# Performance work log

Measured on AMD Instinct MI355X. Metric: run time of the kernel, lower is better.

## Reference

```python
import jax, jax.numpy as jnp
import numpy as np

N = 50000      # nodes
E = 800000     # edges
IN = 128       # in_channels
H = 128        # hidden_channels
OUT = 500      # out_channels
EPS = 1e-5


def setup_inputs() -> dict:
    key = jax.random.key(0)
    ks = jax.random.split(key, 8)
    def rn(k, shape, scale=0.05):
        return jax.random.normal(k, shape, jnp.float32) * scale
    return {
        "x": jax.random.normal(ks[0], (N, IN), jnp.float32),
        "edge_index": jax.random.randint(ks[1], (2, E), 0, N, dtype=jnp.int32),
        "W1": rn(ks[2], (IN, H)), "b1": jnp.zeros((H,), jnp.float32),
        "g1": jnp.ones((H,), jnp.float32), "be1": jnp.zeros((H,), jnp.float32),
        "W2": rn(ks[3], (H, 2 * H)), "b2": jnp.zeros((2 * H,), jnp.float32),
        "g2": jnp.ones((2 * H,), jnp.float32), "be2": jnp.zeros((2 * H,), jnp.float32),
        "W3": rn(ks[4], (2 * H, H)), "b3": jnp.zeros((H,), jnp.float32),
        "g3": jnp.ones((H,), jnp.float32), "be3": jnp.zeros((H,), jnp.float32),
        "Wl1": rn(ks[5], (H, H // 2)), "bl1": jnp.zeros((H // 2,), jnp.float32),
        "g4": jnp.ones((H // 2,), jnp.float32), "be4": jnp.zeros((H // 2,), jnp.float32),
        "Wl2": rn(ks[6], (H // 2, OUT)), "bl2": jnp.zeros((OUT,), jnp.float32),
    }


def layer_norm(x, g, b):
    mu = jnp.mean(x, axis=-1, keepdims=True)
    var = jnp.mean(jnp.square(x - mu), axis=-1, keepdims=True)
    return (x - mu) * jax.lax.rsqrt(var + EPS) * g + b


def gcn_conv(x, W, b, src, dst, n):
    # PyG GCNConv: x' = D^{-1/2} (A + I) D^{-1/2} (x W) + b, with self-loops.
    h = x @ W                                   # [N, F]
    ones = jnp.ones(src.shape[0], h.dtype)
    deg = jax.ops.segment_sum(ones, dst, num_segments=n) + 1.0  # +1 self-loop
    dinv = jnp.where(deg > 0, jax.lax.rsqrt(deg), 0.0)          # [N]
    coef = dinv[src] * dinv[dst]                # [E]
    agg = jax.ops.segment_sum(h[src] * coef[:, None], dst, num_segments=n)
    agg = agg + h * jnp.square(dinv)[:, None]   # self-loop messages
    return agg + b


def reference(x, edge_index, W1, b1, g1, be1, W2, b2, g2, be2,
              W3, b3, g3, be3, Wl1, bl1, g4, be4, Wl2, bl2):
    # eval mode: dropout is identity
    src, dst = edge_index[0], edge_index[1]
    n = x.shape[0]
    h = jax.nn.elu(layer_norm(gcn_conv(x, W1, b1, src, dst, n), g1, be1))
    h = jax.nn.elu(layer_norm(gcn_conv(h, W2, b2, src, dst, n), g2, be2))
    h = jax.nn.elu(layer_norm(gcn_conv(h, W3, b3, src, dst, n), g3, be3))
    h = jax.nn.elu(layer_norm(h @ Wl1 + bl1, g4, be4))
    return h @ Wl2 + bl2
```

## Files before the change

### kernel.cpp

```cpp
#include <hip/hip_runtime.h>
#include <cstdint>


#define LN_EPS 1e-5f

typedef __attribute__((ext_vector_type(8))) short bf16x8;
typedef __attribute__((ext_vector_type(4))) float f32x4;

static __device__ __forceinline__ ushort f2bf(float f) {
  union { float f; uint u; } c; c.f = f;
  uint u = c.u;
  return (ushort)((u + 0x7fffu + ((u >> 16) & 1u)) >> 16);
}
static __device__ __forceinline__ float bf2f(ushort h) {
  union { uint u; float f; } c; c.u = (uint)h << 16;
  return c.f;
}


__global__ void zero1_kernel(int* __restrict__ a, int n) {
  int i = blockIdx.x * blockDim.x + threadIdx.x;
  if (i < n) a[i] = 0;
}

__global__ void deg_kernel(const int* __restrict__ dst, int* __restrict__ deg, int E) {
  int e = blockIdx.x * blockDim.x + threadIdx.x;
  if (e < E) atomicAdd(&deg[dst[e]], 1);
}

__global__ void scan1_kernel(const int* __restrict__ deg, int* __restrict__ excl,
                             int* __restrict__ bsums, float* __restrict__ dinv, int N) {
  __shared__ int s[256];
  int tid = threadIdx.x;
  int i = blockIdx.x * 256 + tid;
  int v = (i < N) ? deg[i] : 0;
  s[tid] = v;
  __syncthreads();
  for (int o = 1; o < 256; o <<= 1) {
    int t = (tid >= o) ? s[tid - o] : 0;
    __syncthreads();
    if (tid >= o) s[tid] += t;
    __syncthreads();
  }
  if (i < N) {
    excl[i] = s[tid] - v;
    dinv[i] = rsqrtf((float)v + 1.0f);
  }
  if (tid == 255) bsums[blockIdx.x] = s[tid];
}

__global__ void scan2_kernel(int* __restrict__ bsums, int nb) {
  __shared__ int s[256];
  int tid = threadIdx.x;
  int v = (tid < nb) ? bsums[tid] : 0;
  s[tid] = v;
  __syncthreads();
  for (int o = 1; o < 256; o <<= 1) {
    int t = (tid >= o) ? s[tid - o] : 0;
    __syncthreads();
    if (tid >= o) s[tid] += t;
    __syncthreads();
  }
  if (tid < nb) bsums[tid] = s[tid] - v;
}

__global__ void scan3_kernel(int* __restrict__ rowptr, int* __restrict__ fill,
                             const int* __restrict__ bsums, int N, int Etotal) {
  int i = blockIdx.x * blockDim.x + threadIdx.x;
  if (i < N) {
    int v = rowptr[i] + bsums[i >> 8];
    rowptr[i] = v;
    fill[i] = v;
  } else if (i == N) {
    rowptr[N] = Etotal;
  }
}

__global__ void fill_kernel(const int* __restrict__ src, const int* __restrict__ dst,
                            int* __restrict__ fill, int* __restrict__ srcs, int E) {
  int e = blockIdx.x * blockDim.x + threadIdx.x;
  if (e >= E) return;
  int idx = atomicAdd(&fill[dst[e]], 1);
  srcs[idx] = src[e];
}


__global__ void f2bf_vec_kernel(const float* __restrict__ in, ushort* __restrict__ out, int n4) {
  int i = blockIdx.x * blockDim.x + threadIdx.x;
  if (i >= n4) return;
  float4 v = ((const float4*)in)[i];
  ushort4 o;
  o.x = f2bf(v.x); o.y = f2bf(v.y); o.z = f2bf(v.z); o.w = f2bf(v.w);
  ((ushort4*)out)[i] = o;
}

struct WConvArgs {
  const float* w[5];
  ushort* wt[5];
  int K[5], N[5];
  int off[6];
};

__global__ void wconv_kernel(WConvArgs a, int total) {
  int i = blockIdx.x * blockDim.x + threadIdx.x;
  if (i >= total) return;
  int m = 0;
  while (i >= a.off[m + 1]) m++;
  int j = i - a.off[m];
  int k = j / a.N[m], n = j - k * a.N[m];
  a.wt[m][(size_t)n * a.K[m] + k] = f2bf(a.w[m][j]);
}

#define TBM 128
#define TBN 128
#define TBK 32
#define LDK 40

template <bool OUT_BF16>
__global__ __launch_bounds__(256, 2) void mfma_gemm_kernel(
    const ushort* __restrict__ A, const ushort* __restrict__ Bt,
    const float* __restrict__ bias, void* __restrict__ Cout,
    int M, int N, int K) {
  __shared__ ushort As[TBM][LDK];
  __shared__ ushort Bs[TBN][LDK];
  const int tid = threadIdx.x;
  const int lane = tid & 63;
  const int w = tid >> 6;
  const int wm = w & 1, wn = w >> 1;
  const int quad = lane >> 4, l16 = lane & 15;
  const int rowBase = blockIdx.y * TBM;
  const int colBase = blockIdx.x * TBN;

  f32x4 acc[4][4] = {};
  const int lr = tid >> 2;
  const int lk = (tid & 3) * 8;

  for (int k0 = 0; k0 < K; k0 += TBK) {
#pragma unroll
    for (int h = 0; h < 2; h++) {
      int r = lr + h * 64;
      int grow = rowBase + r;
      uint4 va = make_uint4(0, 0, 0, 0);
      if (grow < M) va = *(const uint4*)(A + (size_t)grow * K + k0 + lk);
      *(uint4*)&As[r][lk] = va;
      int gcol = colBase + r;
      uint4 vb = make_uint4(0, 0, 0, 0);
      if (gcol < N) vb = *(const uint4*)(Bt + (size_t)gcol * K + k0 + lk);
      *(uint4*)&Bs[r][lk] = vb;
    }
    __syncthreads();
    bf16x8 af[4], bfr[4];
#pragma unroll
    for (int i = 0; i < 4; i++) {
      af[i]  = *(const bf16x8*)&As[wm * 64 + i * 16 + l16][quad * 8];
      bfr[i] = *(const bf16x8*)&Bs[wn * 64 + i * 16 + l16][quad * 8];
    }
#pragma unroll
    for (int i = 0; i < 4; i++)
#pragma unroll
      for (int j = 0; j < 4; j++)
        acc[i][j] = __builtin_amdgcn_mfma_f32_16x16x32_bf16(af[i], bfr[j], acc[i][j], 0, 0, 0);
    __syncthreads();
  }
#pragma unroll
  for (int i = 0; i < 4; i++) {
    int row0 = rowBase + wm * 64 + i * 16 + quad * 4;
#pragma unroll
    for (int j = 0; j < 4; j++) {
      int col = colBase + wn * 64 + j * 16 + l16;
      if (col >= N) continue;
      float bv = bias ? bias[col] : 0.f;
#pragma unroll
      for (int r = 0; r < 4; r++) {
        int row = row0 + r;
        if (row >= M) continue;
        float v = acc[i][j][r] + bv;
        if (OUT_BF16) ((ushort*)Cout)[(size_t)row * N + col] = f2bf(v);
        else          ((float*)Cout)[(size_t)row * N + col] = v;
      }
    }
  }
}


__global__ __launch_bounds__(256) void agg_kernel(
    const ushort* __restrict__ hb, const int* __restrict__ rowptr,
    const int* __restrict__ srcs, const float* __restrict__ dinv,
    uint* __restrict__ out, int Nn) {
  const int wave = threadIdx.x >> 6;
  const int n = blockIdx.x * 4 + wave;
  if (n >= Nn) return;
  const int f = threadIdx.x & 63;
  const uint* h32 = (const uint*)hb;
  const float di = dinv[n];
  uint self = h32[(size_t)n * 64 + f];
  float a0 = bf2f((ushort)(self & 0xffffu)) * di * di;
  float a1 = bf2f((ushort)(self >> 16)) * di * di;
  int i = rowptr[n];
  const int e = rowptr[n + 1];
  for (; i + 3 < e; i += 4) {
    int s0 = srcs[i], s1 = srcs[i + 1], s2 = srcs[i + 2], s3 = srcs[i + 3];
    float c0 = dinv[s0] * di, c1 = dinv[s1] * di, c2 = dinv[s2] * di, c3 = dinv[s3] * di;
    uint v0 = h32[(size_t)s0 * 64 + f];
    uint v1 = h32[(size_t)s1 * 64 + f];
    uint v2 = h32[(size_t)s2 * 64 + f];
    uint v3 = h32[(size_t)s3 * 64 + f];
    a0 += c0 * bf2f((ushort)(v0 & 0xffffu)) + c1 * bf2f((ushort)(v1 & 0xffffu)) +
          c2 * bf2f((ushort)(v2 & 0xffffu)) + c3 * bf2f((ushort)(v3 & 0xffffu));
    a1 += c0 * bf2f((ushort)(v0 >> 16)) + c1 * bf2f((ushort)(v1 >> 16)) +
          c2 * bf2f((ushort)(v2 >> 16)) + c3 * bf2f((ushort)(v3 >> 16));
  }
  for (; i < e; i++) {
    int s = srcs[i];
    float c = dinv[s] * di;
    uint v = h32[(size_t)s * 64 + f];
    a0 += c * bf2f((ushort)(v & 0xffffu));
    a1 += c * bf2f((ushort)(v >> 16));
  }
  out[(size_t)n * 64 + f] = (uint)f2bf(a0) | ((uint)f2bf(a1) << 16);
}

__global__ __launch_bounds__(256) void agg_ln_kernel(
    const ushort* __restrict__ hb, const int* __restrict__ rowptr,
    const int* __restrict__ srcs, const float* __restrict__ dinv,
    const float* __restrict__ bias, const float* __restrict__ g,
    const float* __restrict__ be, uint* __restrict__ out, int Nn) {
  const int wave = threadIdx.x >> 6;
  const int n = blockIdx.x * 4 + wave;
  if (n >= Nn) return;
  const int f = threadIdx.x & 63;
  const uint* h32 = (const uint*)hb;
  const float di = dinv[n];
  uint self = h32[(size_t)n * 64 + f];
  float2 bv = ((const float2*)bias)[f];
  float a0 = bf2f((ushort)(self & 0xffffu)) * di * di + bv.x;
  float a1 = bf2f((ushort)(self >> 16)) * di * di + bv.y;
  int i = rowptr[n];
  const int e = rowptr[n + 1];
  for (; i + 3 < e; i += 4) {
    int s0 = srcs[i], s1 = srcs[i + 1], s2 = srcs[i + 2], s3 = srcs[i + 3];
    float c0 = dinv[s0] * di, c1 = dinv[s1] * di, c2 = dinv[s2] * di, c3 = dinv[s3] * di;
    uint v0 = h32[(size_t)s0 * 64 + f];
    uint v1 = h32[(size_t)s1 * 64 + f];
    uint v2 = h32[(size_t)s2 * 64 + f];
    uint v3 = h32[(size_t)s3 * 64 + f];
    a0 += c0 * bf2f((ushort)(v0 & 0xffffu)) + c1 * bf2f((ushort)(v1 & 0xffffu)) +
          c2 * bf2f((ushort)(v2 & 0xffffu)) + c3 * bf2f((ushort)(v3 & 0xffffu));
    a1 += c0 * bf2f((ushort)(v0 >> 16)) + c1 * bf2f((ushort)(v1 >> 16)) +
          c2 * bf2f((ushort)(v2 >> 16)) + c3 * bf2f((ushort)(v3 >> 16));
  }
  for (; i < e; i++) {
    int s = srcs[i];
    float c = dinv[s] * di;
    uint v = h32[(size_t)s * 64 + f];
    a0 += c * bf2f((ushort)(v & 0xffffu));
    a1 += c * bf2f((ushort)(v >> 16));
  }
  float s = a0 + a1;
#pragma unroll
  for (int o = 32; o >= 1; o >>= 1) s += __shfl_xor(s, o);
  float mean = s * (1.0f / 128.0f);
  float d0 = a0 - mean, d1 = a1 - mean;
  float q = d0 * d0 + d1 * d1;
#pragma unroll
  for (int o = 32; o >= 1; o >>= 1) q += __shfl_xor(q, o);
  float rstd = rsqrtf(q * (1.0f / 128.0f) + LN_EPS);
  float2 gv = ((const float2*)g)[f];
  float2 bev = ((const float2*)be)[f];
  float y0 = d0 * rstd * gv.x + bev.x;
  float y1 = d1 * rstd * gv.y + bev.y;
  y0 = (y0 > 0.f) ? y0 : expm1f(y0);
  y1 = (y1 > 0.f) ? y1 : expm1f(y1);
  out[(size_t)n * 64 + f] = (uint)f2bf(y0) | ((uint)f2bf(y1) << 16);
}

template <int F, bool IN_BF16>
__global__ __launch_bounds__(F) void ln_elu_kernel(const void* __restrict__ xin,
                                                   const float* __restrict__ g,
                                                   const float* __restrict__ be,
                                                   ushort* __restrict__ out) {
  constexpr int NW = (F + 63) / 64;
  __shared__ float sb[NW];
  const int row = blockIdx.x;
  const int f = threadIdx.x;
  float v;
  if (IN_BF16) v = bf2f(((const ushort*)xin)[(size_t)row * F + f]);
  else         v = ((const float*)xin)[(size_t)row * F + f];
  float s = v;
#pragma unroll
  for (int o = 32; o >= 1; o >>= 1) s += __shfl_xor(s, o);
  float mean;
  if constexpr (NW == 1) {
    mean = s * (1.0f / F);
  } else {
    if ((f & 63) == 0) sb[f >> 6] = s;
    __syncthreads();
    float t = 0.f;
#pragma unroll
    for (int w2 = 0; w2 < NW; w2++) t += sb[w2];
    mean = t * (1.0f / F);
    __syncthreads();
  }
  float d = v - mean;
  float q = d * d;
#pragma unroll
  for (int o = 32; o >= 1; o >>= 1) q += __shfl_xor(q, o);
  float var;
  if constexpr (NW == 1) {
    var = q * (1.0f / F);
  } else {
    if ((f & 63) == 0) sb[f >> 6] = q;
    __syncthreads();
    float t = 0.f;
#pragma unroll
    for (int w2 = 0; w2 < NW; w2++) t += sb[w2];
    var = t * (1.0f / F);
  }
  float y = d * rsqrtf(var + LN_EPS) * g[f] + be[f];
  out[(size_t)row * F + f] = f2bf((y > 0.f) ? y : expm1f(y));
}


extern "C" void kernel_launch(void* const* d_in, const int* in_sizes, int n_in,
                              void* d_out, int out_size, void* d_ws, size_t ws_size,
                              hipStream_t stream) {
  const float* x   = (const float*)d_in[0];
  const int*   ei  = (const int*)d_in[1];
  const float* W1  = (const float*)d_in[2];
  const float* b1  = (const float*)d_in[3];
  const float* g1  = (const float*)d_in[4];
  const float* be1 = (const float*)d_in[5];
  const float* W2  = (const float*)d_in[6];
  const float* b2  = (const float*)d_in[7];
  const float* g2  = (const float*)d_in[8];
  const float* be2 = (const float*)d_in[9];
  const float* W3  = (const float*)d_in[10];
  const float* b3  = (const float*)d_in[11];
  const float* g3  = (const float*)d_in[12];
  const float* be3 = (const float*)d_in[13];
  const float* Wl1 = (const float*)d_in[14];
  const float* bl1 = (const float*)d_in[15];
  const float* g4  = (const float*)d_in[16];
  const float* be4 = (const float*)d_in[17];
  const float* Wl2 = (const float*)d_in[18];
  const float* bl2 = (const float*)d_in[19];

  const int N = in_sizes[0] / 128;
  const int E = in_sizes[1] / 2;
  const int* esrc = ei;
  const int* edst = ei + E;

  char* p = (char*)d_ws;
  float* F1 = (float*)p;              p += (size_t)N * 128 * 4;
  ushort* Pb = (ushort*)p;            p += (size_t)N * 256 * 2;
  ushort* Qb = (ushort*)p;            p += (size_t)N * 256 * 2;
  ushort* W1t = (ushort*)p;           p += 128 * 128 * 2;
  ushort* W2t = (ushort*)p;           p += 128 * 256 * 2;
  ushort* W3t = (ushort*)p;           p += 256 * 128 * 2;
  ushort* Wl1t = (ushort*)p;          p += 128 * 64 * 2;
  ushort* Wl2t = (ushort*)p;          p += 64 * 500 * 2;
  int*   srcs  = (int*)p;             p += (size_t)E * 4;
  int*   deg   = (int*)p;             p += (size_t)N * 4;
  float* dinv  = (float*)p;           p += (size_t)N * 4;
  int*   rowptr= (int*)p;             p += (size_t)(N + 2) * 4;
  int*   fill  = (int*)p;             p += (size_t)N * 4;
  int*   bsums = (int*)p;             p += 256 * 4;
  ushort* xb = (ushort*)F1;

  const int nb = (N + 255) / 256;
  const int eb = (E + 255) / 256;

  zero1_kernel<<<nb, 256, 0, stream>>>(deg, N);
  deg_kernel<<<eb, 256, 0, stream>>>(edst, deg, E);
  scan1_kernel<<<nb, 256, 0, stream>>>(deg, rowptr, bsums, dinv, N);
  scan2_kernel<<<1, 256, 0, stream>>>(bsums, nb);
  scan3_kernel<<<(N + 256) / 256, 256, 0, stream>>>(rowptr, fill, bsums, N, E);
  fill_kernel<<<eb, 256, 0, stream>>>(esrc, edst, fill, srcs, E);

  f2bf_vec_kernel<<<(N * 128 / 4 + 255) / 256, 256, 0, stream>>>(x, xb, N * 128 / 4);
  WConvArgs wa;
  wa.w[0] = W1;  wa.wt[0] = W1t;  wa.K[0] = 128; wa.N[0] = 128;
  wa.w[1] = W2;  wa.wt[1] = W2t;  wa.K[1] = 128; wa.N[1] = 256;
  wa.w[2] = W3;  wa.wt[2] = W3t;  wa.K[2] = 256; wa.N[2] = 128;
  wa.w[3] = Wl1; wa.wt[3] = Wl1t; wa.K[3] = 128; wa.N[3] = 64;
  wa.w[4] = Wl2; wa.wt[4] = Wl2t; wa.K[4] = 64;  wa.N[4] = 500;
  wa.off[0] = 0;
  for (int m = 0; m < 5; m++) wa.off[m + 1] = wa.off[m] + wa.K[m] * wa.N[m];
  int wtotal = wa.off[5];
  wconv_kernel<<<(wtotal + 255) / 256, 256, 0, stream>>>(wa, wtotal);

  auto gemm_bf = [&](const ushort* A, const ushort* Bt, const float* bias, ushort* C,
                     int M, int Nn, int K) {
    dim3 grid((Nn + TBN - 1) / TBN, (M + TBM - 1) / TBM);
    mfma_gemm_kernel<true><<<grid, 256, 0, stream>>>(A, Bt, bias, C, M, Nn, K);
  };
  auto gemm_f32 = [&](const ushort* A, const ushort* Bt, const float* bias, float* C,
                      int M, int Nn, int K) {
    dim3 grid((Nn + TBN - 1) / TBN, (M + TBM - 1) / TBM);
    mfma_gemm_kernel<false><<<grid, 256, 0, stream>>>(A, Bt, bias, C, M, Nn, K);
  };
  const int ab = (N + 3) / 4;

  gemm_bf(xb, W1t, nullptr, Pb, N, 128, 128);
  agg_ln_kernel<<<ab, 256, 0, stream>>>(Pb, rowptr, srcs, dinv, b1, g1, be1, (uint*)Qb, N);

  agg_kernel<<<ab, 256, 0, stream>>>(Qb, rowptr, srcs, dinv, (uint*)Pb, N);
  gemm_bf(Pb, W2t, b2, Qb, N, 256, 128);
  ln_elu_kernel<256, true><<<N, 256, 0, stream>>>(Qb, g2, be2, Pb);

  gemm_bf(Pb, W3t, nullptr, Qb, N, 128, 256);
  agg_ln_kernel<<<ab, 256, 0, stream>>>(Qb, rowptr, srcs, dinv, b3, g3, be3, (uint*)Pb, N);

  gemm_f32(Pb, Wl1t, bl1, F1, N, 64, 128);
  ln_elu_kernel<64, false><<<N, 64, 0, stream>>>(F1, g4, be4, Qb);

  gemm_f32(Qb, Wl2t, bl2, (float*)d_out, N, 500, 64);
}
```

Before: 531.0 us.

## Fuse input bf16 cast, LN-ELU epilogue, and scan/zero kernels to cut launches

The first GEMM now reads fp32 x directly and converts to bf16 while staging tiles, which removes the separate conversion kernel and its round trip through memory. The Wl1 GEMM gets a fused LayerNorm+ELU epilogue (64 columns, reduced with 16-lane shuffles), so the fp32 intermediate and the separate ln_elu kernel are gone. The degree zeroing is folded into the weight-conversion kernel, and scan2/scan3 are merged into one kernel in which each block reduces the preceding block sums itself. Together these cut kernel launches and intermediate traffic, at the cost of redundant per-block reductions and half of the waves sitting idle in the fused epilogue.

Measured after the change: 518.7 us. 2.3% less time.

```diff
diff --git a/kernel.cpp b/kernel.cpp
--- a/kernel.cpp
+++ b/kernel.cpp
@@ -17,11 +17,6 @@
   return c.f;
 }
 
-
-__global__ void zero1_kernel(int* __restrict__ a, int n) {
-  int i = blockIdx.x * blockDim.x + threadIdx.x;
-  if (i < n) a[i] = 0;
-}
 
 __global__ void deg_kernel(const int* __restrict__ dst, int* __restrict__ deg, int E) {
   int e = blockIdx.x * blockDim.x + threadIdx.x;
@@ -49,28 +44,24 @@
   if (tid == 255) bsums[blockIdx.x] = s[tid];
 }
 
-__global__ void scan2_kernel(int* __restrict__ bsums, int nb) {
-  __shared__ int s[256];
-  int tid = threadIdx.x;
-  int v = (tid < nb) ? bsums[tid] : 0;
-  s[tid] = v;
+__global__ void scan23_kernel(int* __restrict__ rowptr, int* __restrict__ fill,
+                              const int* __restrict__ bsums, int N, int Etotal, int nb) {
+  __shared__ int sh[256];
+  const int tid = threadIdx.x;
+  const int bix = blockIdx.x;
+  int v = (tid < bix && tid < nb) ? bsums[tid] : 0;
+  sh[tid] = v;
   __syncthreads();
-  for (int o = 1; o < 256; o <<= 1) {
-    int t = (tid >= o) ? s[tid - o] : 0;
-    __syncthreads();
-    if (tid >= o) s[tid] += t;
-    __syncthreads();
-  }
-  if (tid < nb) bsums[tid] = s[tid] - v;
-}
-
-__global__ void scan3_kernel(int* __restrict__ rowptr, int* __restrict__ fill,
-                             const int* __restrict__ bsums, int N, int Etotal) {
-  int i = blockIdx.x * blockDim.x + threadIdx.x;
+  for (int o = 128; o > 0; o >>= 1) {
+    if (tid < o) sh[tid] += sh[tid + o];
+    __syncthreads();
+  }
+  const int off = sh[0];
+  int i = bix * 256 + tid;
   if (i < N) {
-    int v = rowptr[i] + bsums[i >> 8];
-    rowptr[i] = v;
-    fill[i] = v;
+    int r = rowptr[i] + off;
+    rowptr[i] = r;
+    fill[i] = r;
   } else if (i == N) {
     rowptr[N] = Etotal;
   }
@@ -85,15 +76,6 @@
 }
 
 
-__global__ void f2bf_vec_kernel(const float* __restrict__ in, ushort* __restrict__ out, int n4) {
-  int i = blockIdx.x * blockDim.x + threadIdx.x;
-  if (i >= n4) return;
-  float4 v = ((const float4*)in)[i];
-  ushort4 o;
-  o.x = f2bf(v.x); o.y = f2bf(v.y); o.z = f2bf(v.z); o.w = f2bf(v.w);
-  ((ushort4*)out)[i] = o;
-}
-
 struct WConvArgs {
   const float* w[5];
   ushort* wt[5];
@@ -101,8 +83,9 @@
   int off[6];
 };
 
-__global__ void wconv_kernel(WConvArgs a, int total) {
+__global__ void prep_kernel(WConvArgs a, int total, int* __restrict__ deg, int Nn) {
   int i = blockIdx.x * blockDim.x + threadIdx.x;
+  if (i < Nn) deg[i] = 0;
   if (i >= total) return;
   int m = 0;
   while (i >= a.off[m + 1]) m++;
@@ -116,10 +99,11 @@
 #define TBK 32
 #define LDK 40
 
-template <bool OUT_BF16>
+template <int AF32, int EMODE>
 __global__ __launch_bounds__(256, 2) void mfma_gemm_kernel(
-    const ushort* __restrict__ A, const ushort* __restrict__ Bt,
-    const float* __restrict__ bias, void* __restrict__ Cout,
+    const void* __restrict__ A, const ushort* __restrict__ Bt,
+    const float* __restrict__ bias, const float* __restrict__ gamma,
+    const float* __restrict__ beta, void* __restrict__ Cout,
     int M, int N, int K) {
   __shared__ ushort As[TBM][LDK];
   __shared__ ushort Bs[TBN][LDK];
@@ -140,9 +124,26 @@
     for (int h = 0; h < 2; h++) {
       int r = lr + h * 64;
       int grow = rowBase + r;
-      uint4 va = make_uint4(0, 0, 0, 0);
-      if (grow < M) va = *(const uint4*)(A + (size_t)grow * K + k0 + lk);
-      *(uint4*)&As[r][lk] = va;
+      if (AF32) {
+        const float* Af = (const float*)A;
+        float4 v0 = make_float4(0.f, 0.f, 0.f, 0.f), v1 = v0;
+        if (grow < M) {
+          const float* ap = Af + (size_t)grow * K + k0 + lk;
+          v0 = *(const float4*)ap;
+          v1 = *(const float4*)(ap + 4);
+        }
+        uint4 wv;
+        wv.x = (uint)f2bf(v0.x) | ((uint)f2bf(v0.y) << 16);
+        wv.y = (uint)f2bf(v0.z) | ((uint)f2bf(v0.w) << 16);
+        wv.z = (uint)f2bf(v1.x) | ((uint)f2bf(v1.y) << 16);
+        wv.w = (uint)f2bf(v1.z) | ((uint)f2bf(v1.w) << 16);
+        *(uint4*)&As[r][lk] = wv;
+      } else {
+        const ushort* Ab = (const ushort*)A;
+        uint4 va = make_uint4(0, 0, 0, 0);
+        if (grow < M) va = *(const uint4*)(Ab + (size_t)grow * K + k0 + lk);
+        *(uint4*)&As[r][lk] = va;
+      }
       int gcol = colBase + r;
       uint4 vb = make_uint4(0, 0, 0, 0);
       if (gcol < N) vb = *(const uint4*)(Bt + (size_t)gcol * K + k0 + lk);
@@ -162,21 +163,64 @@
         acc[i][j] = __builtin_amdgcn_mfma_f32_16x16x32_bf16(af[i], bfr[j], acc[i][j], 0, 0, 0);
     __syncthreads();
   }
-#pragma unroll
-  for (int i = 0; i < 4; i++) {
-    int row0 = rowBase + wm * 64 + i * 16 + quad * 4;
-#pragma unroll
-    for (int j = 0; j < 4; j++) {
-      int col = colBase + wn * 64 + j * 16 + l16;
-      if (col >= N) continue;
-      float bv = bias ? bias[col] : 0.f;
+
+  if constexpr (EMODE == 2) {
+    if (wn != 0) return;
+    const int rowB = rowBase + wm * 64;
+#pragma unroll
+    for (int i = 0; i < 4; i++) {
 #pragma unroll
       for (int r = 0; r < 4; r++) {
-        int row = row0 + r;
-        if (row >= M) continue;
-        float v = acc[i][j][r] + bv;
-        if (OUT_BF16) ((ushort*)Cout)[(size_t)row * N + col] = f2bf(v);
-        else          ((float*)Cout)[(size_t)row * N + col] = v;
+        int row = rowB + i * 16 + quad * 4 + r;
+        float v[4];
+        float s = 0.f;
+#pragma unroll
+        for (int j = 0; j < 4; j++) {
+          int col = j * 16 + l16;
+          v[j] = acc[i][j][r] + bias[col];
+          s += v[j];
+        }
+#pragma unroll
+        for (int o = 8; o >= 1; o >>= 1) s += __shfl_xor(s, o, 16);
+        float mean = s * (1.0f / 64.0f);
+        float q = 0.f;
+#pragma unroll
+        for (int j = 0; j < 4; j++) {
+          float d = v[j] - mean;
+          q += d * d;
+        }
+#pragma unroll
+        for (int o = 8; o >= 1; o >>= 1) q += __shfl_xor(q, o, 16);
+        float rstd = rsqrtf(q * (1.0f / 64.0f) + LN_EPS);
+        if (row < M) {
+#pragma unroll
+          for (int j = 0; j < 4; j++) {
+            int col = j * 16 + l16;
+            float y = (v[j] - mean) * rstd * gamma[col] + beta[col];
+            y = (y > 0.f) ? y : expm1f(y);
+            ((ushort*)Cout)[(size_t)row * 64 + col] = f2bf(y);
+          }
+        }
+      }
+    }
+    return;
+  } else {
+#pragma unroll
+    for (int i = 0; i < 4; i++) {
+      int row0 = rowBase + wm * 64 + i * 16 + quad * 4;
+#pragma unroll
+      for (int j = 0; j < 4; j++) {
+        int col = colBase + wn * 64 + j * 16 + l16;
+        if (col >= N) continue;
+        float bv = bias ? bias[col] : 0.f;
+#pragma unroll
+        for (int r = 0; r < 4; r++) {
+          int row = row0 + r;
+          if (row >= M) continue;
+          float vv = acc[i][j][r] + bv;
+          if (EMODE == 1) ((ushort*)Cout)[(size_t)row * N + col] = f2bf(vv);
+          else            ((float*)Cout)[(size_t)row * N + col] = vv;
+        }
       }
     }
   }
@@ -351,7 +395,6 @@
   const int* edst = ei + E;
 
   char* p = (char*)d_ws;
-  float* F1 = (float*)p;              p += (size_t)N * 128 * 4;
   ushort* Pb = (ushort*)p;            p += (size_t)N * 256 * 2;
   ushort* Qb = (ushort*)p;            p += (size_t)N * 256 * 2;
   ushort* W1t = (ushort*)p;           p += 128 * 128 * 2;
@@ -365,19 +408,10 @@
   int*   rowptr= (int*)p;             p += (size_t)(N + 2) * 4;
   int*   fill  = (int*)p;             p += (size_t)N * 4;
   int*   bsums = (int*)p;             p += 256 * 4;
-  ushort* xb = (ushort*)F1;
 
   const int nb = (N + 255) / 256;
   const int eb = (E + 255) / 256;
 
-  zero1_kernel<<<nb, 256, 0, stream>>>(deg, N);
-  deg_kernel<<<eb, 256, 0, stream>>>(edst, deg, E);
-  scan1_kernel<<<nb, 256, 0, stream>>>(deg, rowptr, bsums, dinv, N);
-  scan2_kernel<<<1, 256, 0, stream>>>(bsums, nb);
-  scan3_kernel<<<(N + 256) / 256, 256, 0, stream>>>(rowptr, fill, bsums, N, E);
-  fill_kernel<<<eb, 256, 0, stream>>>(esrc, edst, fill, srcs, E);
-
-  f2bf_vec_kernel<<<(N * 128 / 4 + 255) / 256, 256, 0, stream>>>(x, xb, N * 128 / 4);
   WConvArgs wa;
   wa.w[0] = W1;  wa.wt[0] = W1t;  wa.K[0] = 128; wa.N[0] = 128;
   wa.w[1] = W2;  wa.wt[1] = W2t;  wa.K[1] = 128; wa.N[1] = 256;
@@ -387,32 +421,35 @@
   wa.off[0] = 0;
   for (int m = 0; m < 5; m++) wa.off[m + 1] = wa.off[m] + wa.K[m] * wa.N[m];
   int wtotal = wa.off[5];
-  wconv_kernel<<<(wtotal + 255) / 256, 256, 0, stream>>>(wa, wtotal);
-
-  auto gemm_bf = [&](const ushort* A, const ushort* Bt, const float* bias, ushort* C,
-                     int M, int Nn, int K) {
-    dim3 grid((Nn + TBN - 1) / TBN, (M + TBM - 1) / TBM);
-    mfma_gemm_kernel<true><<<grid, 256, 0, stream>>>(A, Bt, bias, C, M, Nn, K);
+  int ptotal = wtotal > N ? wtotal : N;
+  prep_kernel<<<(ptotal + 255) / 256, 256, 0, stream>>>(wa, wtotal, deg, N);
+
+  deg_kernel<<<eb, 256, 0, stream>>>(edst, deg, E);
+  scan1_kernel<<<nb, 256, 0, stream>>>(deg, rowptr, bsums, dinv, N);
+  scan23_kernel<<<(N + 256) / 256, 256, 0, stream>>>(rowptr, fill, bsums, N, E, nb);
+  fill_kernel<<<eb, 256, 0, stream>>>(esrc, edst, fill, srcs, E);
+
+  const int ab = (N + 3) / 4;
+  auto grid_of = [&](int M, int Nn) {
+    return dim3((Nn + TBN - 1) / TBN, (M + TBM - 1) / TBM);
   };
-  auto gemm_f32 = [&](const ushort* A, const ushort* Bt, const float* bias, float* C,
-                      int M, int Nn, int K) {
-    dim3 grid((Nn + TBN - 1) / TBN, (M + TBM - 1) / TBM);
-    mfma_gemm_kernel<false><<<grid, 256, 0, stream>>>(A, Bt, bias, C, M, Nn, K);
-  };
-  const int ab = (N + 3) / 4;
-
-  gemm_bf(xb, W1t, nullptr, Pb, N, 128, 128);
+
+  mfma_gemm_kernel<1, 1><<<grid_of(N, 128), 256, 0, stream>>>(
+      x, W1t, nullptr, nullptr, nullptr, Pb, N, 128, 128);
   agg_ln_kernel<<<ab, 256, 0, stream>>>(Pb, rowptr, srcs, dinv, b1, g1, be1, (uint*)Qb, N);
 
   agg_kernel<<<ab, 256, 0, stream>>>(Qb, rowptr, srcs, dinv, (uint*)Pb, N);
-  gemm_bf(Pb, W2t, b2, Qb, N, 256, 128);
+  mfma_gemm_kernel<0, 1><<<grid_of(N, 256), 256, 0, stream>>>(
+      Pb, W2t, b2, nullptr, nullptr, Qb, N, 256, 128);
   ln_elu_kernel<256, true><<<N, 256, 0, stream>>>(Qb, g2, be2, Pb);
 
-  gemm_bf(Pb, W3t, nullptr, Qb, N, 128, 256);
+  mfma_gemm_kernel<0, 1><<<grid_of(N, 128), 256, 0, stream>>>(
+      Pb, W3t, nullptr, nullptr, nullptr, Qb, N, 128, 256);
   agg_ln_kernel<<<ab, 256, 0, stream>>>(Qb, rowptr, srcs, dinv, b3, g3, be3, (uint*)Pb, N);
 
-  gemm_f32(Pb, Wl1t, bl1, F1, N, 64, 128);
-  ln_elu_kernel<64, false><<<N, 64, 0, stream>>>(F1, g4, be4, Qb);
-
-  gemm_f32(Qb, Wl2t, bl2, (float*)d_out, N, 500, 64);
-}
+  mfma_gemm_kernel<0, 2><<<grid_of(N, 64), 256, 0, stream>>>(
+      Pb, Wl1t, bl1, g4, be4, Qb, N, 64, 128);
+
+  mfma_gemm_kernel<0, 0><<<grid_of(N, 500), 256, 0, stream>>>(
+      Qb, Wl2t, bl2, nullptr, nullptr, d_out, N, 500, 64);
+}
```
